# Kernel optimization log

Measured on AMD Instinct MI355X. Metric: run time of the kernel, lower is better.

Reference implementation:

```python
import jax, jax.numpy as jnp
import numpy as np


def setup_inputs() -> dict:
    key = jax.random.key(0)
    k1, k2, k3, k4 = jax.random.split(key, 4)
    B, W, S, C, h, w = 8, 5, 5, 640, 10, 10  # episodes, n_way, n_shot, channels, feat HxW
    Q = 75  # queries per episode
    return {
        "x_shot": jax.random.normal(k1, (B, W, S, C, h, w), dtype=jnp.float32),
        "x_query": jax.random.normal(k2, (B, Q, C, h, w), dtype=jnp.float32),
        "r_cos": jax.random.normal(k3, (1,), dtype=jnp.float32),
        "r_dn4": jax.random.normal(k4, (1,), dtype=jnp.float32),
        "neighbor_k": 5,
    }


def reference(x_shot, x_query, r_cos, r_dn4, neighbor_k):
    B, W, S, C, h, w = x_shot.shape
    Q = x_query.shape[1]
    hw = h * w

    base = x_shot.reshape(B, W, S, C, hw)            # [B,W,S,C,hw]
    query = x_query.reshape(B, Q, C, hw)             # [B,Q,C,hw]

    # --- cosine prototype branch ---
    base_mean = base.mean(axis=4)                    # [B,W,S,C] GAP
    proto = base_mean.mean(axis=2)                   # [B,W,C]
    q_mean = query.mean(axis=3)                      # [B,Q,C]
    qn = q_mean / jnp.linalg.norm(q_mean, axis=-1, keepdims=True)
    pn = proto / jnp.linalg.norm(proto, axis=-1, keepdims=True)
    logits_cos = jnp.einsum('bqc,bwc->bqw', qn, pn)  # [B,Q,W]

    # --- DN4 local-descriptor branch ---
    # support descriptors: [B,W,S*hw,C]
    base_mix = jnp.transpose(base, (0, 1, 2, 4, 3)).reshape(B, W, S * hw, C)
    # NOTE: original code normalizes support along the DESCRIPTOR axis (dim 0 of [S*hw,C]),
    # i.e. per-channel across descriptors. Reproduce that faithfully.
    sup = base_mix / jnp.linalg.norm(base_mix, axis=2, keepdims=True)
    # query descriptors: [B,Q,hw,C], L2-normalized per descriptor (over C)
    qd = jnp.transpose(query, (0, 1, 3, 2))
    qd = qd / jnp.linalg.norm(qd, axis=-1, keepdims=True)

    # patch-wise similarity: [B,Q,W,hw,S*hw]
    sim = jnp.einsum('bqpc,bwdc->bqwpd', qd, sup)
    topv, _ = jax.lax.top_k(sim, neighbor_k)         # [B,Q,W,hw,k]
    # original: sum over ALL (hw rows x k) top values, divided by neighbor_k
    logits_dn4 = topv.sum(axis=(-1, -2)) / neighbor_k  # [B,Q,W]

    return r_cos * logits_cos + r_dn4 * logits_dn4
```

## Files before the change

kernel.cpp:

```cpp
#include <hip/hip_runtime.h>
#include <cstddef>

typedef unsigned short u16;
typedef _Float16 f16x8 __attribute__((ext_vector_type(8)));
typedef float f32x4 __attribute__((ext_vector_type(4)));

#define NB  8
#define NW  5
#define NS  5
#define NC  640
#define NHW 100
#define NQ  75
#define ND  500
#define NDP 512
#define NR  7500
#define NRP 7552
#define NRT 59

#define OFF_SUP   ((size_t)0)
#define OFF_ABF   ((size_t)26214400)
#define OFF_QRN   ((size_t)103546880)
#define OFF_PROTO ((size_t)103788544)

__device__ __forceinline__ u16 f2h_bits(float x) {
  _Float16 h = (_Float16)x;
  return __builtin_bit_cast(u16, h);
}
__device__ __forceinline__ float h2f_bits(u16 u) {
  return (float)__builtin_bit_cast(_Float16, u);
}

__device__ __forceinline__ float block_sum(float v, float* sc, int t) {
  v += __shfl_xor(v, 32, 64);
  v += __shfl_xor(v, 16, 64);
  v += __shfl_xor(v, 8, 64);
  v += __shfl_xor(v, 4, 64);
  v += __shfl_xor(v, 2, 64);
  v += __shfl_xor(v, 1, 64);
  __syncthreads();
  if ((t & 63) == 0) sc[t >> 6] = v;
  __syncthreads();
  return sc[0] + sc[1] + sc[2] + sc[3];
}

__device__ __forceinline__ void t5_insert(float (&t5)[5], float v) {
  if (v > t5[0]) {
    t5[0] = v; float tmp;
    if (t5[0] > t5[1]) { tmp = t5[0]; t5[0] = t5[1]; t5[1] = tmp; }
    if (t5[1] > t5[2]) { tmp = t5[1]; t5[1] = t5[2]; t5[2] = tmp; }
    if (t5[2] > t5[3]) { tmp = t5[2]; t5[2] = t5[3]; t5[3] = tmp; }
    if (t5[3] > t5[4]) { tmp = t5[3]; t5[3] = t5[4]; t5[4] = tmp; }
  }
}

__global__ __launch_bounds__(256) void k1_sup(const float* __restrict__ xs,
                                              u16* __restrict__ sup2,
                                              float* __restrict__ proto_g) {
  const int cc = blockIdx.x, w = blockIdx.y, b = blockIdx.z;
  const int t = threadIdx.x;
  __shared__ u16 tile[512 * 34];
  __shared__ float rn[32];
  const size_t bw = (size_t)b * NW + w;
  const float* xbase = xs + bw * NS * NC * NHW;
  const int cb = cc * 32;

  for (int s = 0; s < NS; s++) {
    const float4* rb = (const float4*)(xbase + ((size_t)s * NC + cb) * NHW);
    for (int i4 = t; i4 < 800; i4 += 256) {
      const float4 v = rb[i4];
      const int c = i4 / 25, p4 = i4 % 25;
      const int d = s * NHW + p4 * 4;
      tile[(d    ) * 34 + c] = f2h_bits(v.x);
      tile[(d + 1) * 34 + c] = f2h_bits(v.y);
      tile[(d + 2) * 34 + c] = f2h_bits(v.z);
      tile[(d + 3) * 34 + c] = f2h_bits(v.w);
    }
  }
  if (t < 384) tile[(500 + (t >> 5)) * 34 + (t & 31)] = 0;
  __syncthreads();
  {
    const int c = t >> 3, part = t & 7;
    float ss = 0.f, sm = 0.f;
    for (int d = part; d < ND; d += 8) {
      const float x = h2f_bits(tile[d * 34 + c]);
      ss += x * x; sm += x;
    }
    ss += __shfl_xor(ss, 1, 64); ss += __shfl_xor(ss, 2, 64); ss += __shfl_xor(ss, 4, 64);
    sm += __shfl_xor(sm, 1, 64); sm += __shfl_xor(sm, 2, 64); sm += __shfl_xor(sm, 4, 64);
    if (part == 0) {
      rn[c] = 1.0f / sqrtf(ss);
      proto_g[bw * NC + cb + c] = sm;
    }
  }
  __syncthreads();
  u16* obase = sup2 + bw * NDP * NC + cb;
  for (int idx = t; idx < 512 * 32; idx += 256) {
    const int cl = idx & 31, d = idx >> 5;
    obase[(size_t)d * NC + cl] = f2h_bits(h2f_bits(tile[d * 34 + cl]) * rn[cl]);
  }
}

__global__ __launch_bounds__(256) void k2_query(const float* __restrict__ xq,
                                                const float* __restrict__ proto_g,
                                                const float* __restrict__ rcosp,
                                                u16* __restrict__ Abf,
                                                float* __restrict__ qrn,
                                                float* __restrict__ out) {
  const int q = blockIdx.x, b = blockIdx.y;
  const int t = threadIdx.x;
  __shared__ u16 tile[128 * 106];
  __shared__ float qm[NC];
  __shared__ float qs[NHW];
  __shared__ float sc[4];
  const float* xbase = xq + ((size_t)b * NQ + q) * NC * NHW;
  u16* abase = Abf + ((size_t)b * NRP + (size_t)q * NHW) * NC;

  if (t < NHW) qs[t] = 0.f;
  __syncthreads();

  for (int cc = 0; cc < 5; cc++) {
    const float4* rb = (const float4*)(xbase + (size_t)cc * 128 * NHW);
    for (int i4 = t; i4 < 3200; i4 += 256) {
      const float4 xv = rb[i4];
      const int e = i4 * 4;
      const int p = e % NHW, cl = e / NHW;
      const unsigned lo = (unsigned)f2h_bits(xv.x) | ((unsigned)f2h_bits(xv.y) << 16);
      const unsigned hi = (unsigned)f2h_bits(xv.z) | ((unsigned)f2h_bits(xv.w) << 16);
      unsigned* tw = (unsigned*)&tile[cl * 106 + p];
      tw[0] = lo; tw[1] = hi;
    }
    __syncthreads();
    if (t < 128) {
      float s = 0.f;
      const unsigned* row = (const unsigned*)&tile[t * 106];
      for (int j = 0; j < 50; j++) {
        const unsigned u = row[j];
        s += h2f_bits((u16)(u & 0xffffu)) + h2f_bits((u16)(u >> 16));
      }
      qm[cc * 128 + t] = s;
    } else if (t < 228) {
      const int p = t - 128;
      float s = 0.f;
      for (int c = 0; c < 128; c++) {
        const float x = h2f_bits(tile[c * 106 + p]);
        s += x * x;
      }
      qs[p] += s;
    }
    {
      const int c0 = t & 63, pr = t >> 6;
      for (int p = pr; p < NHW; p += 4) {
        abase[(size_t)p * NC + cc * 128 + c0]      = tile[c0 * 106 + p];
        abase[(size_t)p * NC + cc * 128 + c0 + 64] = tile[(c0 + 64) * 106 + p];
      }
    }
    __syncthreads();
  }
  if (t < NHW) qrn[(size_t)b * NRP + q * NHW + t] = 1.0f / sqrtf(qs[t]);

  float part = 0.f;
  for (int c = t; c < NC; c += 256) part += qm[c] * qm[c];
  const float qq = block_sum(part, sc, t);
  const float rcos = rcosp[0];
  for (int w = 0; w < NW; w++) {
    const float* pr_ = proto_g + ((size_t)b * NW + w) * NC;
    float dp = 0.f, pp = 0.f;
    for (int c = t; c < NC; c += 256) { const float pv = pr_[c]; dp += qm[c] * pv; pp += pv * pv; }
    dp = block_sum(dp, sc, t);
    pp = block_sum(pp, sc, t);
    if (t == 0) out[((size_t)b * NQ + q) * NW + w] = rcos * dp / sqrtf(qq * pp);
  }
  if (q == 0) {
    u16* pz = Abf + ((size_t)b * NRP + NR) * NC;
    for (int i = t; i < (NRP - NR) * NC; i += 256) pz[i] = 0;
  }
}

__global__ __launch_bounds__(256, 3) void k4_dn4(const u16* __restrict__ Abf,
                                                 const u16* __restrict__ sup2,
                                                 const float* __restrict__ qrn,
                                                 const float* __restrict__ rdn4p,
                                                 const int* __restrict__ nkp,
                                                 float* __restrict__ out) {
  const int rt = blockIdx.x, w = blockIdx.y, b = blockIdx.z;
  const int t = threadIdx.x;
  const int lane = t & 63, wid = t >> 6;
  const int m = lane & 15, quad = lane >> 4;
  const int wx = wid & 1, wy = wid >> 1;

  __shared__ __align__(16) u16 stg[2][2][128 * 40];

  const u16* Ab = Abf + ((size_t)b * NRP + (size_t)rt * 128) * NC;
  const u16* Bb = sup2 + ((size_t)b * NW + w) * NDP * NC;

  const int rr = t >> 2;
  const int c8 = (t & 3) * 8;

  uint4 ra0, ra1, rb0, rb1;

#define G_LOAD2(CT_, K0_) do {                                            \
    const u16* ap_ = Ab + (size_t)rr * NC + (K0_) + c8;                   \
    ra0 = *(const uint4*)ap_;                                             \
    ra1 = *(const uint4*)(ap_ + (size_t)64 * NC);                         \
    const u16* bp_ = Bb + (size_t)((CT_) * 128 + rr) * NC + (K0_) + c8;   \
    rb0 = *(const uint4*)bp_;                                             \
    rb1 = *(const uint4*)(bp_ + (size_t)64 * NC);                         \
  } while (0)

#define LDS_STORE(BUF_) do {                                              \
    *(uint4*)&stg[BUF_][0][rr * 40 + c8]        = ra0;                    \
    *(uint4*)&stg[BUF_][0][(rr + 64) * 40 + c8] = ra1;                    \
    *(uint4*)&stg[BUF_][1][rr * 40 + c8]        = rb0;                    \
    *(uint4*)&stg[BUF_][1][(rr + 64) * 40 + c8] = rb1;                    \
  } while (0)

  float t5[4][5];
#pragma unroll
  for (int qt = 0; qt < 4; qt++)
#pragma unroll
    for (int i = 0; i < 5; i++) t5[qt][i] = -3e38f;

  G_LOAD2(0, 0);
  LDS_STORE(0);
  G_LOAD2(0, 32);
  __syncthreads();

  for (int ct = 0; ct < 4; ct++) {
    f32x4 acc[4][4];
#pragma unroll
    for (int dt = 0; dt < 4; dt++)
#pragma unroll
      for (int qt = 0; qt < 4; qt++)
        acc[dt][qt] = (f32x4){0.f, 0.f, 0.f, 0.f};

    for (int s = 0; s < 20; s++) {
      if (!(ct == 3 && s == 19)) LDS_STORE((s + 1) & 1);
      if (!(ct == 3 && s >= 18)) {
        const int ctn = (s < 18) ? ct : ct + 1;
        const int k0n = ((s < 18) ? (s + 2) : (s - 18)) * 32;
        G_LOAD2(ctn, k0n);
      }
      {
        const u16* la = &stg[s & 1][0][0];
        const u16* lb = &stg[s & 1][1][0];
        f16x8 af0, af1, af2, af3, bf0, bf1, bf2, bf3;
        af0 = *(const f16x8*)&la[(wy * 64 +  0 + m) * 40 + quad * 8];
        af1 = *(const f16x8*)&la[(wy * 64 + 16 + m) * 40 + quad * 8];
        af2 = *(const f16x8*)&la[(wy * 64 + 32 + m) * 40 + quad * 8];
        af3 = *(const f16x8*)&la[(wy * 64 + 48 + m) * 40 + quad * 8];
        bf0 = *(const f16x8*)&lb[(wx * 64 +  0 + m) * 40 + quad * 8];
        bf1 = *(const f16x8*)&lb[(wx * 64 + 16 + m) * 40 + quad * 8];
        bf2 = *(const f16x8*)&lb[(wx * 64 + 32 + m) * 40 + quad * 8];
        bf3 = *(const f16x8*)&lb[(wx * 64 + 48 + m) * 40 + quad * 8];
        acc[0][0] = __builtin_amdgcn_mfma_f32_16x16x32_f16(bf0, af0, acc[0][0], 0, 0, 0);
        acc[0][1] = __builtin_amdgcn_mfma_f32_16x16x32_f16(bf0, af1, acc[0][1], 0, 0, 0);
        acc[0][2] = __builtin_amdgcn_mfma_f32_16x16x32_f16(bf0, af2, acc[0][2], 0, 0, 0);
        acc[0][3] = __builtin_amdgcn_mfma_f32_16x16x32_f16(bf0, af3, acc[0][3], 0, 0, 0);
        acc[1][0] = __builtin_amdgcn_mfma_f32_16x16x32_f16(bf1, af0, acc[1][0], 0, 0, 0);
        acc[1][1] = __builtin_amdgcn_mfma_f32_16x16x32_f16(bf1, af1, acc[1][1], 0, 0, 0);
        acc[1][2] = __builtin_amdgcn_mfma_f32_16x16x32_f16(bf1, af2, acc[1][2], 0, 0, 0);
        acc[1][3] = __builtin_amdgcn_mfma_f32_16x16x32_f16(bf1, af3, acc[1][3], 0, 0, 0);
        acc[2][0] = __builtin_amdgcn_mfma_f32_16x16x32_f16(bf2, af0, acc[2][0], 0, 0, 0);
        acc[2][1] = __builtin_amdgcn_mfma_f32_16x16x32_f16(bf2, af1, acc[2][1], 0, 0, 0);
        acc[2][2] = __builtin_amdgcn_mfma_f32_16x16x32_f16(bf2, af2, acc[2][2], 0, 0, 0);
        acc[2][3] = __builtin_amdgcn_mfma_f32_16x16x32_f16(bf2, af3, acc[2][3], 0, 0, 0);
        acc[3][0] = __builtin_amdgcn_mfma_f32_16x16x32_f16(bf3, af0, acc[3][0], 0, 0, 0);
        acc[3][1] = __builtin_amdgcn_mfma_f32_16x16x32_f16(bf3, af1, acc[3][1], 0, 0, 0);
        acc[3][2] = __builtin_amdgcn_mfma_f32_16x16x32_f16(bf3, af2, acc[3][2], 0, 0, 0);
        acc[3][3] = __builtin_amdgcn_mfma_f32_16x16x32_f16(bf3, af3, acc[3][3], 0, 0, 0);
      }
      __syncthreads();
    }

    const int dlim = ND - ct * 128 - wx * 64;
    if (dlim >= 64) {
#pragma unroll
      for (int dt = 0; dt < 4; dt++)
#pragma unroll
        for (int qt = 0; qt < 4; qt++)
#pragma unroll
          for (int r = 0; r < 4; r++)
            t5_insert(t5[qt], acc[dt][qt][r]);
    } else {
#pragma unroll
      for (int dt = 0; dt < 4; dt++)
#pragma unroll
        for (int qt = 0; qt < 4; qt++)
#pragma unroll
          for (int r = 0; r < 4; r++)
            if (dt * 16 + quad * 4 + r < dlim) t5_insert(t5[qt], acc[dt][qt][r]);
    }
  }

#pragma unroll
  for (int qt = 0; qt < 4; qt++) {
    float rec[5];
#pragma unroll
    for (int i = 0; i < 5; i++) rec[i] = __shfl_xor(t5[qt][i], 16, 64);
#pragma unroll
    for (int i = 0; i < 5; i++) t5_insert(t5[qt], rec[i]);
#pragma unroll
    for (int i = 0; i < 5; i++) rec[i] = __shfl_xor(t5[qt][i], 32, 64);
#pragma unroll
    for (int i = 0; i < 5; i++) t5_insert(t5[qt], rec[i]);
  }

  float* scratch = (float*)&stg[0][0][0];
  if (wx == 1 && quad == 0) {
#pragma unroll
    for (int qt = 0; qt < 4; qt++) {
      const int row = wy * 64 + qt * 16 + m;
#pragma unroll
      for (int i = 0; i < 5; i++) scratch[row * 5 + i] = t5[qt][i];
    }
  }
  __syncthreads();
  if (wx == 0 && quad == 0) {
    const float scale = rdn4p[0] / (float)nkp[0];
#pragma unroll
    for (int qt = 0; qt < 4; qt++) {
      const int row = wy * 64 + qt * 16 + m;
#pragma unroll
      for (int i = 0; i < 5; i++) t5_insert(t5[qt], scratch[row * 5 + i]);
      const int r = rt * 128 + row;
      if (r < NR) {
        const float s = t5[qt][0] + t5[qt][1] + t5[qt][2] + t5[qt][3] + t5[qt][4];
        const float contrib = s * qrn[(size_t)b * NRP + r] * scale;
        const int qi = r / NHW;
        atomicAdd(&out[((size_t)b * NQ + qi) * NW + w], contrib);
      }
    }
  }
#undef G_LOAD2
#undef LDS_STORE
}

extern "C" void kernel_launch(void* const* d_in, const int* in_sizes, int n_in,
                              void* d_out, int out_size, void* d_ws, size_t ws_size,
                              hipStream_t stream) {
  (void)in_sizes; (void)n_in; (void)out_size; (void)ws_size;
  const float* xs   = (const float*)d_in[0];
  const float* xq   = (const float*)d_in[1];
  const float* rcos = (const float*)d_in[2];
  const float* rdn4 = (const float*)d_in[3];
  const int*   nk   = (const int*)d_in[4];
  float* out = (float*)d_out;
  char* ws = (char*)d_ws;
  u16*   sup2  = (u16*)(ws + OFF_SUP);
  u16*   Abf   = (u16*)(ws + OFF_ABF);
  float* qrn   = (float*)(ws + OFF_QRN);
  float* proto = (float*)(ws + OFF_PROTO);

  k1_sup <<<dim3(20, NW, NB),  dim3(256), 0, stream>>>(xs, sup2, proto);
  k2_query<<<dim3(NQ, NB),     dim3(256), 0, stream>>>(xq, proto, rcos, Abf, qrn, out);
  k4_dn4 <<<dim3(NRT, NW, NB), dim3(256), 0, stream>>>(Abf, sup2, qrn, rdn4, nk, out);
}
```

Baseline: 508.7 us.

## Deepen global prefetch to two slabs and use fragment-ordered LDS layout

The DN4 GEMM kernel now keeps two register sets of prefetched global data, so loads run two k-slabs ahead instead of one, hiding more memory latency behind the MFMAs. The LDS staging layout also changes from a padded row-major tile (stride 40) to a linear, fragment-ordered layout. Each thread stores and reads contiguous 16-byte chunks, which removes the address arithmetic and is meant to avoid bank conflicts. The cost is extra VGPRs for the second prefetch set, which could hurt occupancy under launch_bounds(256,3).

After: 595.8 us. 1.17x slower.

```diff
diff --git a/kernel.cpp b/kernel.cpp
--- a/kernel.cpp
+++ b/kernel.cpp
@@ -188,42 +188,102 @@
   const int m = lane & 15, quad = lane >> 4;
   const int wx = wid & 1, wy = wid >> 1;
 
-  __shared__ __align__(16) u16 stg[2][2][128 * 40];
+  __shared__ __align__(16) u16 stg[2][2][4096];
 
   const u16* Ab = Abf + ((size_t)b * NRP + (size_t)rt * 128) * NC;
   const u16* Bb = sup2 + ((size_t)b * NW + w) * NDP * NC;
 
-  const int rr = t >> 2;
-  const int c8 = (t & 3) * 8;
-
-  uint4 ra0, ra1, rb0, rb1;
-
-#define G_LOAD2(CT_, K0_) do {                                            \
-    const u16* ap_ = Ab + (size_t)rr * NC + (K0_) + c8;                   \
-    ra0 = *(const uint4*)ap_;                                             \
-    ra1 = *(const uint4*)(ap_ + (size_t)64 * NC);                         \
-    const u16* bp_ = Bb + (size_t)((CT_) * 128 + rr) * NC + (K0_) + c8;   \
-    rb0 = *(const uint4*)bp_;                                             \
-    rb1 = *(const uint4*)(bp_ + (size_t)64 * NC);                         \
+  const int row0 = ((t >> 6) << 4) | (t & 15);
+  const int qc = (t >> 4) & 3;
+  const size_t aoff = (size_t)row0 * NC + qc * 8;
+  const size_t a64 = (size_t)64 * NC;
+  const int tt8 = t * 8;
+  const int lane8 = lane * 8;
+  const int wyo = wy * 2048, wxo = wx * 2048;
+
+  uint4 pA0, pA1, pB0, pB1;
+  uint4 qA0, qA1, qB0, qB1;
+
+  float t5[4][5];
+#pragma unroll
+  for (int qt = 0; qt < 4; qt++)
+#pragma unroll
+    for (int i = 0; i < 5; i++) t5[qt][i] = -3e38f;
+
+  {
+    const u16* ap = Ab + aoff;
+    pA0 = *(const uint4*)ap;
+    pA1 = *(const uint4*)(ap + a64);
+    const u16* bp = Bb + aoff;
+    pB0 = *(const uint4*)bp;
+    pB1 = *(const uint4*)(bp + a64);
+    *(uint4*)&stg[0][0][tt8]        = pA0;
+    *(uint4*)&stg[0][0][tt8 + 2048] = pA1;
+    *(uint4*)&stg[0][1][tt8]        = pB0;
+    *(uint4*)&stg[0][1][tt8 + 2048] = pB1;
+    pA0 = *(const uint4*)(ap + 32);
+    pA1 = *(const uint4*)(ap + a64 + 32);
+    pB0 = *(const uint4*)(bp + 32);
+    pB1 = *(const uint4*)(bp + a64 + 32);
+    qA0 = *(const uint4*)(ap + 64);
+    qA1 = *(const uint4*)(ap + a64 + 64);
+    qB0 = *(const uint4*)(bp + 64);
+    qB1 = *(const uint4*)(bp + a64 + 64);
+  }
+  __syncthreads();
+
+  const float* qrb = qrn + (size_t)b * NRP;
+
+#define SLAB_ITER(S_, RA0_, RA1_, RB0_, RB1_) do {                          \
+    if (!(ct == 3 && (S_) == 19)) {                                         \
+      u16* sa_ = &stg[((S_) + 1) & 1][0][0];                                \
+      *(uint4*)&sa_[tt8]        = RA0_;                                     \
+      *(uint4*)&sa_[tt8 + 2048] = RA1_;                                     \
+      u16* sb_ = &stg[((S_) + 1) & 1][1][0];                                \
+      *(uint4*)&sb_[tt8]        = RB0_;                                     \
+      *(uint4*)&sb_[tt8 + 2048] = RB1_;                                     \
+    }                                                                       \
+    if (!(ct == 3 && (S_) >= 17)) {                                         \
+      const int ct3_ = ((S_) < 17) ? ct : ct + 1;                           \
+      const int k0_  = (((S_) < 17) ? ((S_) + 3) : ((S_) - 17)) * 32;       \
+      const u16* ap_ = Ab + aoff + k0_;                                     \
+      RA0_ = *(const uint4*)ap_;                                            \
+      RA1_ = *(const uint4*)(ap_ + a64);                                    \
+      const u16* bp_ = Bb + (size_t)ct3_ * (128 * NC) + aoff + k0_;         \
+      RB0_ = *(const uint4*)bp_;                                            \
+      RB1_ = *(const uint4*)(bp_ + a64);                                    \
+    }                                                                       \
+    {                                                                       \
+      const u16* la_ = &stg[(S_) & 1][0][wyo];                              \
+      const u16* lb_ = &stg[(S_) & 1][1][wxo];                              \
+      f16x8 af0, af1, af2, af3, bf0, bf1, bf2, bf3;                         \
+      af0 = *(const f16x8*)&la_[lane8];                                     \
+      af1 = *(const f16x8*)&la_[lane8 + 512];                               \
+      af2 = *(const f16x8*)&la_[lane8 + 1024];                              \
+      af3 = *(const f16x8*)&la_[lane8 + 1536];                              \
+      bf0 = *(const f16x8*)&lb_[lane8];                                     \
+      bf1 = *(const f16x8*)&lb_[lane8 + 512];                               \
+      bf2 = *(const f16x8*)&lb_[lane8 + 1024];                              \
+      bf3 = *(const f16x8*)&lb_[lane8 + 1536];                              \
+      acc[0][0] = __builtin_amdgcn_mfma_f32_16x16x32_f16(bf0, af0, acc[0][0], 0, 0, 0); \
+      acc[0][1] = __builtin_amdgcn_mfma_f32_16x16x32_f16(bf0, af1, acc[0][1], 0, 0, 0); \
+      acc[0][2] = __builtin_amdgcn_mfma_f32_16x16x32_f16(bf0, af2, acc[0][2], 0, 0, 0); \
+      acc[0][3] = __builtin_amdgcn_mfma_f32_16x16x32_f16(bf0, af3, acc[0][3], 0, 0, 0); \
+      acc[1][0] = __builtin_amdgcn_mfma_f32_16x16x32_f16(bf1, af0, acc[1][0], 0, 0, 0); \
+      acc[1][1] = __builtin_amdgcn_mfma_f32_16x16x32_f16(bf1, af1, acc[1][1], 0, 0, 0); \
+      acc[1][2] = __builtin_amdgcn_mfma_f32_16x16x32_f16(bf1, af2, acc[1][2], 0, 0, 0); \
+      acc[1][3] = __builtin_amdgcn_mfma_f32_16x16x32_f16(bf1, af3, acc[1][3], 0, 0, 0); \
+      acc[2][0] = __builtin_amdgcn_mfma_f32_16x16x32_f16(bf2, af0, acc[2][0], 0, 0, 0); \
+      acc[2][1] = __builtin_amdgcn_mfma_f32_16x16x32_f16(bf2, af1, acc[2][1], 0, 0, 0); \
+      acc[2][2] = __builtin_amdgcn_mfma_f32_16x16x32_f16(bf2, af2, acc[2][2], 0, 0, 0); \
+      acc[2][3] = __builtin_amdgcn_mfma_f32_16x16x32_f16(bf2, af3, acc[2][3], 0, 0, 0); \
+      acc[3][0] = __builtin_amdgcn_mfma_f32_16x16x32_f16(bf3, af0, acc[3][0], 0, 0, 0); \
+      acc[3][1] = __builtin_amdgcn_mfma_f32_16x16x32_f16(bf3, af1, acc[3][1], 0, 0, 0); \
+      acc[3][2] = __builtin_amdgcn_mfma_f32_16x16x32_f16(bf3, af2, acc[3][2], 0, 0, 0); \
+      acc[3][3] = __builtin_amdgcn_mfma_f32_16x16x32_f16(bf3, af3, acc[3][3], 0, 0, 0); \
+    }                                                                       \
+    __syncthreads();                                                        \
   } while (0)
-
-#define LDS_STORE(BUF_) do {                                              \
-    *(uint4*)&stg[BUF_][0][rr * 40 + c8]        = ra0;                    \
-    *(uint4*)&stg[BUF_][0][(rr + 64) * 40 + c8] = ra1;                    \
-    *(uint4*)&stg[BUF_][1][rr * 40 + c8]        = rb0;                    \
-    *(uint4*)&stg[BUF_][1][(rr + 64) * 40 + c8] = rb1;                    \
-  } while (0)
-
-  float t5[4][5];
-#pragma unroll
-  for (int qt = 0; qt < 4; qt++)
-#pragma unroll
-    for (int i = 0; i < 5; i++) t5[qt][i] = -3e38f;
-
-  G_LOAD2(0, 0);
-  LDS_STORE(0);
-  G_LOAD2(0, 32);
-  __syncthreads();
 
   for (int ct = 0; ct < 4; ct++) {
     f32x4 acc[4][4];
@@ -233,43 +293,9 @@
       for (int qt = 0; qt < 4; qt++)
         acc[dt][qt] = (f32x4){0.f, 0.f, 0.f, 0.f};
 
-    for (int s = 0; s < 20; s++) {
-      if (!(ct == 3 && s == 19)) LDS_STORE((s + 1) & 1);
-      if (!(ct == 3 && s >= 18)) {
-        const int ctn = (s < 18) ? ct : ct + 1;
-        const int k0n = ((s < 18) ? (s + 2) : (s - 18)) * 32;
-        G_LOAD2(ctn, k0n);
-      }
-      {
-        const u16* la = &stg[s & 1][0][0];
-        const u16* lb = &stg[s & 1][1][0];
-        f16x8 af0, af1, af2, af3, bf0, bf1, bf2, bf3;
-        af0 = *(const f16x8*)&la[(wy * 64 +  0 + m) * 40 + quad * 8];
-        af1 = *(const f16x8*)&la[(wy * 64 + 16 + m) * 40 + quad * 8];
-        af2 = *(const f16x8*)&la[(wy * 64 + 32 + m) * 40 + quad * 8];
-        af3 = *(const f16x8*)&la[(wy * 64 + 48 + m) * 40 + quad * 8];
-        bf0 = *(const f16x8*)&lb[(wx * 64 +  0 + m) * 40 + quad * 8];
-        bf1 = *(const f16x8*)&lb[(wx * 64 + 16 + m) * 40 + quad * 8];
-        bf2 = *(const f16x8*)&lb[(wx * 64 + 32 + m) * 40 + quad * 8];
-        bf3 = *(const f16x8*)&lb[(wx * 64 + 48 + m) * 40 + quad * 8];
-        acc[0][0] = __builtin_amdgcn_mfma_f32_16x16x32_f16(bf0, af0, acc[0][0], 0, 0, 0);
-        acc[0][1] = __builtin_amdgcn_mfma_f32_16x16x32_f16(bf0, af1, acc[0][1], 0, 0, 0);
-        acc[0][2] = __builtin_amdgcn_mfma_f32_16x16x32_f16(bf0, af2, acc[0][2], 0, 0, 0);
-        acc[0][3] = __builtin_amdgcn_mfma_f32_16x16x32_f16(bf0, af3, acc[0][3], 0, 0, 0);
-        acc[1][0] = __builtin_amdgcn_mfma_f32_16x16x32_f16(bf1, af0, acc[1][0], 0, 0, 0);
-        acc[1][1] = __builtin_amdgcn_mfma_f32_16x16x32_f16(bf1, af1, acc[1][1], 0, 0, 0);
-        acc[1][2] = __builtin_amdgcn_mfma_f32_16x16x32_f16(bf1, af2, acc[1][2], 0, 0, 0);
-        acc[1][3] = __builtin_amdgcn_mfma_f32_16x16x32_f16(bf1, af3, acc[1][3], 0, 0, 0);
-        acc[2][0] = __builtin_amdgcn_mfma_f32_16x16x32_f16(bf2, af0, acc[2][0], 0, 0, 0);
-        acc[2][1] = __builtin_amdgcn_mfma_f32_16x16x32_f16(bf2, af1, acc[2][1], 0, 0, 0);
-        acc[2][2] = __builtin_amdgcn_mfma_f32_16x16x32_f16(bf2, af2, acc[2][2], 0, 0, 0);
-        acc[2][3] = __builtin_amdgcn_mfma_f32_16x16x32_f16(bf2, af3, acc[2][3], 0, 0, 0);
-        acc[3][0] = __builtin_amdgcn_mfma_f32_16x16x32_f16(bf3, af0, acc[3][0], 0, 0, 0);
-        acc[3][1] = __builtin_amdgcn_mfma_f32_16x16x32_f16(bf3, af1, acc[3][1], 0, 0, 0);
-        acc[3][2] = __builtin_amdgcn_mfma_f32_16x16x32_f16(bf3, af2, acc[3][2], 0, 0, 0);
-        acc[3][3] = __builtin_amdgcn_mfma_f32_16x16x32_f16(bf3, af3, acc[3][3], 0, 0, 0);
-      }
-      __syncthreads();
+    for (int s = 0; s < 20; s += 2) {
+      SLAB_ITER(s,     pA0, pA1, pB0, pB1);
+      SLAB_ITER(s + 1, qA0, qA1, qB0, qB1);
     }
 
     const int dlim = ND - ct * 128 - wx * 64;
@@ -291,6 +317,7 @@
             if (dt * 16 + quad * 4 + r < dlim) t5_insert(t5[qt], acc[dt][qt][r]);
     }
   }
+#undef SLAB_ITER
 
 #pragma unroll
   for (int qt = 0; qt < 4; qt++) {
@@ -325,14 +352,12 @@
       const int r = rt * 128 + row;
       if (r < NR) {
         const float s = t5[qt][0] + t5[qt][1] + t5[qt][2] + t5[qt][3] + t5[qt][4];
-        const float contrib = s * qrn[(size_t)b * NRP + r] * scale;
+        const float contrib = s * qrb[r] * scale;
         const int qi = r / NHW;
         atomicAdd(&out[((size_t)b * NQ + qi) * NW + w], contrib);
       }
     }
   }
-#undef G_LOAD2
-#undef LDS_STORE
 }
 
 extern "C" void kernel_launch(void* const* d_in, const int* in_sizes, int n_in,
```

## Use direct global-to-LDS loads with triple-buffered pipeline in DN4 GEMM

Applied to the files above, without the earlier changes.

Replaces the register-staged global loads and LDS stores in the DN4 similarity GEMM with global_load_lds direct-to-LDS copies. Staging becomes triple-buffered, synchronised by vmcnt waits and raw s_barrier. The LDS layout changes from padded row-major to fragment-ordered 16x32 tiles, so each lane reads its MFMA operand contiguously. This removes the VGPR staging and LDS write instructions and lets loads overlap compute more deeply, but it relies on correct vmcnt accounting. LDS use rises slightly (3x2x4096 u16 = 48 KiB).

Result: slower. 562.6 us (+10.6%).

```diff
diff --git a/kernel.cpp b/kernel.cpp
--- a/kernel.cpp
+++ b/kernel.cpp
@@ -29,6 +29,19 @@
 __device__ __forceinline__ float h2f_bits(u16 u) {
   return (float)__builtin_bit_cast(_Float16, u);
 }
+
+__device__ __forceinline__ void gload_lds16(const u16* g, u16* l) {
+  __builtin_amdgcn_global_load_lds(
+      (const __attribute__((address_space(1))) unsigned int*)g,
+      (__attribute__((address_space(3))) unsigned int*)l,
+      16, 0, 0);
+}
+
+#define S_VMCNT4() asm volatile("s_waitcnt vmcnt(4)" ::: "memory")
+#define S_VMCNT0() asm volatile("s_waitcnt vmcnt(0)" ::: "memory")
+#define S_BAR() do { __builtin_amdgcn_sched_barrier(0);          \
+                     asm volatile("s_barrier" ::: "memory");     \
+                     __builtin_amdgcn_sched_barrier(0); } while (0)
 
 __device__ __forceinline__ float block_sum(float v, float* sc, int t) {
   v += __shfl_xor(v, 32, 64);
@@ -188,43 +201,40 @@
   const int m = lane & 15, quad = lane >> 4;
   const int wx = wid & 1, wy = wid >> 1;
 
-  __shared__ __align__(16) u16 stg[2][2][128 * 40];
+  __shared__ __align__(16) u16 stg[3][2][4096];
 
   const u16* Ab = Abf + ((size_t)b * NRP + (size_t)rt * 128) * NC;
   const u16* Bb = sup2 + ((size_t)b * NW + w) * NDP * NC;
 
-  const int rr = t >> 2;
-  const int c8 = (t & 3) * 8;
-
-  uint4 ra0, ra1, rb0, rb1;
-
-#define G_LOAD2(CT_, K0_) do {                                            \
-    const u16* ap_ = Ab + (size_t)rr * NC + (K0_) + c8;                   \
-    ra0 = *(const uint4*)ap_;                                             \
-    ra1 = *(const uint4*)(ap_ + (size_t)64 * NC);                         \
-    const u16* bp_ = Bb + (size_t)((CT_) * 128 + rr) * NC + (K0_) + c8;   \
-    rb0 = *(const uint4*)bp_;                                             \
-    rb1 = *(const uint4*)(bp_ + (size_t)64 * NC);                         \
+  const size_t go0 = (size_t)(wid * 16 + m) * NC + (size_t)quad * 8;
+  const size_t go1 = (size_t)((wid + 4) * 16 + m) * NC + (size_t)quad * 8;
+  const int l0 = wid * 512 + lane * 8;
+  const int l1 = (wid + 4) * 512 + lane * 8;
+  const int lane8 = lane * 8;
+  const int wyo = wy * 2048, wxo = wx * 2048;
+
+#define ISSUE(BN_, CT_, K0_) do {                                         \
+    const size_t bO_ = (size_t)(CT_) * (128 * NC) + (K0_);                \
+    u16* s0_ = &stg[BN_][0][0];                                           \
+    u16* s1_ = &stg[BN_][1][0];                                           \
+    gload_lds16(Ab + go0 + (K0_), s0_ + l0);                              \
+    gload_lds16(Ab + go1 + (K0_), s0_ + l1);                              \
+    gload_lds16(Bb + bO_ + go0,   s1_ + l0);                              \
+    gload_lds16(Bb + bO_ + go1,   s1_ + l1);                              \
   } while (0)
 
-#define LDS_STORE(BUF_) do {                                              \
-    *(uint4*)&stg[BUF_][0][rr * 40 + c8]        = ra0;                    \
-    *(uint4*)&stg[BUF_][0][(rr + 64) * 40 + c8] = ra1;                    \
-    *(uint4*)&stg[BUF_][1][rr * 40 + c8]        = rb0;                    \
-    *(uint4*)&stg[BUF_][1][(rr + 64) * 40 + c8] = rb1;                    \
-  } while (0)
-
   float t5[4][5];
 #pragma unroll
   for (int qt = 0; qt < 4; qt++)
 #pragma unroll
     for (int i = 0; i < 5; i++) t5[qt][i] = -3e38f;
 
-  G_LOAD2(0, 0);
-  LDS_STORE(0);
-  G_LOAD2(0, 32);
-  __syncthreads();
-
+  ISSUE(0, 0, 0);
+  ISSUE(1, 0, 32);
+  S_VMCNT4();
+  S_BAR();
+
+  int bcur = 0;
   for (int ct = 0; ct < 4; ct++) {
     f32x4 acc[4][4];
 #pragma unroll
@@ -234,24 +244,24 @@
         acc[dt][qt] = (f32x4){0.f, 0.f, 0.f, 0.f};
 
     for (int s = 0; s < 20; s++) {
-      if (!(ct == 3 && s == 19)) LDS_STORE((s + 1) & 1);
+      int b2 = bcur - 1; if (b2 < 0) b2 += 3;
       if (!(ct == 3 && s >= 18)) {
         const int ctn = (s < 18) ? ct : ct + 1;
         const int k0n = ((s < 18) ? (s + 2) : (s - 18)) * 32;
-        G_LOAD2(ctn, k0n);
+        ISSUE(b2, ctn, k0n);
       }
       {
-        const u16* la = &stg[s & 1][0][0];
-        const u16* lb = &stg[s & 1][1][0];
+        const u16* la_ = &stg[bcur][0][wyo];
+        const u16* lb_ = &stg[bcur][1][wxo];
         f16x8 af0, af1, af2, af3, bf0, bf1, bf2, bf3;
-        af0 = *(const f16x8*)&la[(wy * 64 +  0 + m) * 40 + quad * 8];
-        af1 = *(const f16x8*)&la[(wy * 64 + 16 + m) * 40 + quad * 8];
-        af2 = *(const f16x8*)&la[(wy * 64 + 32 + m) * 40 + quad * 8];
-        af3 = *(const f16x8*)&la[(wy * 64 + 48 + m) * 40 + quad * 8];
-        bf0 = *(const f16x8*)&lb[(wx * 64 +  0 + m) * 40 + quad * 8];
-        bf1 = *(const f16x8*)&lb[(wx * 64 + 16 + m) * 40 + quad * 8];
-        bf2 = *(const f16x8*)&lb[(wx * 64 + 32 + m) * 40 + quad * 8];
-        bf3 = *(const f16x8*)&lb[(wx * 64 + 48 + m) * 40 + quad * 8];
+        af0 = *(const f16x8*)&la_[lane8];
+        af1 = *(const f16x8*)&la_[lane8 + 512];
+        af2 = *(const f16x8*)&la_[lane8 + 1024];
+        af3 = *(const f16x8*)&la_[lane8 + 1536];
+        bf0 = *(const f16x8*)&lb_[lane8];
+        bf1 = *(const f16x8*)&lb_[lane8 + 512];
+        bf2 = *(const f16x8*)&lb_[lane8 + 1024];
+        bf3 = *(const f16x8*)&lb_[lane8 + 1536];
         acc[0][0] = __builtin_amdgcn_mfma_f32_16x16x32_f16(bf0, af0, acc[0][0], 0, 0, 0);
         acc[0][1] = __builtin_amdgcn_mfma_f32_16x16x32_f16(bf0, af1, acc[0][1], 0, 0, 0);
         acc[0][2] = __builtin_amdgcn_mfma_f32_16x16x32_f16(bf0, af2, acc[0][2], 0, 0, 0);
@@ -269,7 +279,9 @@
         acc[3][2] = __builtin_amdgcn_mfma_f32_16x16x32_f16(bf3, af2, acc[3][2], 0, 0, 0);
         acc[3][3] = __builtin_amdgcn_mfma_f32_16x16x32_f16(bf3, af3, acc[3][3], 0, 0, 0);
       }
-      __syncthreads();
+      if (ct == 3 && s >= 18) { S_VMCNT0(); } else { S_VMCNT4(); }
+      S_BAR();
+      bcur++; if (bcur == 3) bcur = 0;
     }
 
     const int dlim = ND - ct * 128 - wx * 64;
@@ -291,6 +303,7 @@
             if (dt * 16 + quad * 4 + r < dlim) t5_insert(t5[qt], acc[dt][qt][r]);
     }
   }
+#undef ISSUE
 
 #pragma unroll
   for (int qt = 0; qt < 4; qt++) {
@@ -317,6 +330,7 @@
   __syncthreads();
   if (wx == 0 && quad == 0) {
     const float scale = rdn4p[0] / (float)nkp[0];
+    const float* qrb = qrn + (size_t)b * NRP;
 #pragma unroll
     for (int qt = 0; qt < 4; qt++) {
       const int row = wy * 64 + qt * 16 + m;
@@ -325,14 +339,12 @@
       const int r = rt * 128 + row;
       if (r < NR) {
         const float s = t5[qt][0] + t5[qt][1] + t5[qt][2] + t5[qt][3] + t5[qt][4];
-        const float contrib = s * qrn[(size_t)b * NRP + r] * scale;
+        const float contrib = s * qrb[r] * scale;
         const int qi = r / NHW;
         atomicAdd(&out[((size_t)b * NQ + qi) * NW + w], contrib);
       }
     }
   }
-#undef G_LOAD2
-#undef LDS_STORE
 }
 
 extern "C" void kernel_launch(void* const* d_in, const int* in_sizes, int n_in,
```

## Replace LDS-staged 4-wave DN4 GEMM with single-wave direct-global MFMA tiles

Applied to the files above, without the earlier changes.

The DN4 similarity kernel drops its shared-memory double-buffered 128x128 tile with four waves and __syncthreads. Each block is now one wave computing a 64-row by 128-descriptor tile, loading MFMA fragments straight from global memory. The cross-wave top-5 merge through LDS also goes away. This removes barriers and LDS traffic but gives up cross-wave operand reuse, so every fragment comes from global or L2, and the loads are strided per lane, so coalescing suffers.

Result: slower. 894.0 us (+75.7%).

```diff
diff --git a/kernel.cpp b/kernel.cpp
--- a/kernel.cpp
+++ b/kernel.cpp
@@ -15,7 +15,7 @@
 #define NDP 512
 #define NR  7500
 #define NRP 7552
-#define NRT 59
+#define NRU 118
 
 #define OFF_SUP   ((size_t)0)
 #define OFF_ABF   ((size_t)26214400)
@@ -176,43 +176,19 @@
   }
 }
 
-__global__ __launch_bounds__(256, 3) void k4_dn4(const u16* __restrict__ Abf,
-                                                 const u16* __restrict__ sup2,
-                                                 const float* __restrict__ qrn,
-                                                 const float* __restrict__ rdn4p,
-                                                 const int* __restrict__ nkp,
-                                                 float* __restrict__ out) {
-  const int rt = blockIdx.x, w = blockIdx.y, b = blockIdx.z;
-  const int t = threadIdx.x;
-  const int lane = t & 63, wid = t >> 6;
+__global__ __launch_bounds__(64, 2) void k4_dn4(const u16* __restrict__ Abf,
+                                                const u16* __restrict__ sup2,
+                                                const float* __restrict__ qrn,
+                                                const float* __restrict__ rdn4p,
+                                                const int* __restrict__ nkp,
+                                                float* __restrict__ out) {
+  const int ru = blockIdx.x, w = blockIdx.y, b = blockIdx.z;
+  const int lane = threadIdx.x & 63;
   const int m = lane & 15, quad = lane >> 4;
-  const int wx = wid & 1, wy = wid >> 1;
-
-  __shared__ __align__(16) u16 stg[2][2][128 * 40];
-
-  const u16* Ab = Abf + ((size_t)b * NRP + (size_t)rt * 128) * NC;
-  const u16* Bb = sup2 + ((size_t)b * NW + w) * NDP * NC;
-
-  const int rr = t >> 2;
-  const int c8 = (t & 3) * 8;
-
-  uint4 ra0, ra1, rb0, rb1;
-
-#define G_LOAD2(CT_, K0_) do {                                            \
-    const u16* ap_ = Ab + (size_t)rr * NC + (K0_) + c8;                   \
-    ra0 = *(const uint4*)ap_;                                             \
-    ra1 = *(const uint4*)(ap_ + (size_t)64 * NC);                         \
-    const u16* bp_ = Bb + (size_t)((CT_) * 128 + rr) * NC + (K0_) + c8;   \
-    rb0 = *(const uint4*)bp_;                                             \
-    rb1 = *(const uint4*)(bp_ + (size_t)64 * NC);                         \
-  } while (0)
-
-#define LDS_STORE(BUF_) do {                                              \
-    *(uint4*)&stg[BUF_][0][rr * 40 + c8]        = ra0;                    \
-    *(uint4*)&stg[BUF_][0][(rr + 64) * 40 + c8] = ra1;                    \
-    *(uint4*)&stg[BUF_][1][rr * 40 + c8]        = rb0;                    \
-    *(uint4*)&stg[BUF_][1][(rr + 64) * 40 + c8] = rb1;                    \
-  } while (0)
+  const int r0 = ru * 64;
+
+  const u16* Aw = Abf + ((size_t)b * NRP + r0 + m) * NC + quad * 8;
+  const u16* Bw = sup2 + (((size_t)b * NW + w) * NDP + m) * NC + quad * 8;
 
   float t5[4][5];
 #pragma unroll
@@ -220,75 +196,39 @@
 #pragma unroll
     for (int i = 0; i < 5; i++) t5[qt][i] = -3e38f;
 
-  G_LOAD2(0, 0);
-  LDS_STORE(0);
-  G_LOAD2(0, 32);
-  __syncthreads();
-
-  for (int ct = 0; ct < 4; ct++) {
-    f32x4 acc[4][4];
-#pragma unroll
-    for (int dt = 0; dt < 4; dt++)
+  for (int dc = 0; dc < 4; dc++) {
+    const u16* Bc = Bw + (size_t)dc * 128 * NC;
+    f32x4 acc[8][4];
+#pragma unroll
+    for (int dt = 0; dt < 8; dt++)
 #pragma unroll
       for (int qt = 0; qt < 4; qt++)
         acc[dt][qt] = (f32x4){0.f, 0.f, 0.f, 0.f};
 
-    for (int s = 0; s < 20; s++) {
-      if (!(ct == 3 && s == 19)) LDS_STORE((s + 1) & 1);
-      if (!(ct == 3 && s >= 18)) {
-        const int ctn = (s < 18) ? ct : ct + 1;
-        const int k0n = ((s < 18) ? (s + 2) : (s - 18)) * 32;
-        G_LOAD2(ctn, k0n);
-      }
-      {
-        const u16* la = &stg[s & 1][0][0];
-        const u16* lb = &stg[s & 1][1][0];
-        f16x8 af0, af1, af2, af3, bf0, bf1, bf2, bf3;
-        af0 = *(const f16x8*)&la[(wy * 64 +  0 + m) * 40 + quad * 8];
-        af1 = *(const f16x8*)&la[(wy * 64 + 16 + m) * 40 + quad * 8];
-        af2 = *(const f16x8*)&la[(wy * 64 + 32 + m) * 40 + quad * 8];
-        af3 = *(const f16x8*)&la[(wy * 64 + 48 + m) * 40 + quad * 8];
-        bf0 = *(const f16x8*)&lb[(wx * 64 +  0 + m) * 40 + quad * 8];
-        bf1 = *(const f16x8*)&lb[(wx * 64 + 16 + m) * 40 + quad * 8];
-        bf2 = *(const f16x8*)&lb[(wx * 64 + 32 + m) * 40 + quad * 8];
-        bf3 = *(const f16x8*)&lb[(wx * 64 + 48 + m) * 40 + quad * 8];
-        acc[0][0] = __builtin_amdgcn_mfma_f32_16x16x32_f16(bf0, af0, acc[0][0], 0, 0, 0);
-        acc[0][1] = __builtin_amdgcn_mfma_f32_16x16x32_f16(bf0, af1, acc[0][1], 0, 0, 0);
-        acc[0][2] = __builtin_amdgcn_mfma_f32_16x16x32_f16(bf0, af2, acc[0][2], 0, 0, 0);
-        acc[0][3] = __builtin_amdgcn_mfma_f32_16x16x32_f16(bf0, af3, acc[0][3], 0, 0, 0);
-        acc[1][0] = __builtin_amdgcn_mfma_f32_16x16x32_f16(bf1, af0, acc[1][0], 0, 0, 0);
-        acc[1][1] = __builtin_amdgcn_mfma_f32_16x16x32_f16(bf1, af1, acc[1][1], 0, 0, 0);
-        acc[1][2] = __builtin_amdgcn_mfma_f32_16x16x32_f16(bf1, af2, acc[1][2], 0, 0, 0);
-        acc[1][3] = __builtin_amdgcn_mfma_f32_16x16x32_f16(bf1, af3, acc[1][3], 0, 0, 0);
-        acc[2][0] = __builtin_amdgcn_mfma_f32_16x16x32_f16(bf2, af0, acc[2][0], 0, 0, 0);
-        acc[2][1] = __builtin_amdgcn_mfma_f32_16x16x32_f16(bf2, af1, acc[2][1], 0, 0, 0);
-        acc[2][2] = __builtin_amdgcn_mfma_f32_16x16x32_f16(bf2, af2, acc[2][2], 0, 0, 0);
-        acc[2][3] = __builtin_amdgcn_mfma_f32_16x16x32_f16(bf2, af3, acc[2][3], 0, 0, 0);
-        acc[3][0] = __builtin_amdgcn_mfma_f32_16x16x32_f16(bf3, af0, acc[3][0], 0, 0, 0);
-        acc[3][1] = __builtin_amdgcn_mfma_f32_16x16x32_f16(bf3, af1, acc[3][1], 0, 0, 0);
-        acc[3][2] = __builtin_amdgcn_mfma_f32_16x16x32_f16(bf3, af2, acc[3][2], 0, 0, 0);
-        acc[3][3] = __builtin_amdgcn_mfma_f32_16x16x32_f16(bf3, af3, acc[3][3], 0, 0, 0);
-      }
-      __syncthreads();
-    }
-
-    const int dlim = ND - ct * 128 - wx * 64;
-    if (dlim >= 64) {
-#pragma unroll
-      for (int dt = 0; dt < 4; dt++)
+    for (int ks = 0; ks < 20; ks++) {
+      const int k = ks * 32;
+      f16x8 af[4], bf[8];
+#pragma unroll
+      for (int qt = 0; qt < 4; qt++)
+        af[qt] = *(const f16x8*)(Aw + (size_t)qt * (16 * NC) + k);
+#pragma unroll
+      for (int dt = 0; dt < 8; dt++)
+        bf[dt] = *(const f16x8*)(Bc + (size_t)dt * (16 * NC) + k);
+#pragma unroll
+      for (int dt = 0; dt < 8; dt++)
 #pragma unroll
         for (int qt = 0; qt < 4; qt++)
-#pragma unroll
-          for (int r = 0; r < 4; r++)
-            t5_insert(t5[qt], acc[dt][qt][r]);
-    } else {
-#pragma unroll
-      for (int dt = 0; dt < 4; dt++)
-#pragma unroll
-        for (int qt = 0; qt < 4; qt++)
-#pragma unroll
-          for (int r = 0; r < 4; r++)
-            if (dt * 16 + quad * 4 + r < dlim) t5_insert(t5[qt], acc[dt][qt][r]);
+          acc[dt][qt] = __builtin_amdgcn_mfma_f32_16x16x32_f16(bf[dt], af[qt], acc[dt][qt], 0, 0, 0);
+    }
+
+#pragma unroll
+    for (int dt = 0; dt < 8; dt++) {
+      const bool tail = (dc == 3 && dt == 7);
+#pragma unroll
+      for (int qt = 0; qt < 4; qt++)
+#pragma unroll
+        for (int r = 0; r < 4; r++)
+          if (!tail || quad == 0) t5_insert(t5[qt], acc[dt][qt][r]);
     }
   }
 
@@ -305,34 +245,20 @@
     for (int i = 0; i < 5; i++) t5_insert(t5[qt], rec[i]);
   }
 
-  float* scratch = (float*)&stg[0][0][0];
-  if (wx == 1 && quad == 0) {
+  if (quad == 0) {
+    const float scale = rdn4p[0] / (float)nkp[0];
+    const float* qrb = qrn + (size_t)b * NRP;
 #pragma unroll
     for (int qt = 0; qt < 4; qt++) {
-      const int row = wy * 64 + qt * 16 + m;
-#pragma unroll
-      for (int i = 0; i < 5; i++) scratch[row * 5 + i] = t5[qt][i];
-    }
-  }
-  __syncthreads();
-  if (wx == 0 && quad == 0) {
-    const float scale = rdn4p[0] / (float)nkp[0];
-#pragma unroll
-    for (int qt = 0; qt < 4; qt++) {
-      const int row = wy * 64 + qt * 16 + m;
-#pragma unroll
-      for (int i = 0; i < 5; i++) t5_insert(t5[qt], scratch[row * 5 + i]);
-      const int r = rt * 128 + row;
+      const int r = r0 + qt * 16 + m;
       if (r < NR) {
         const float s = t5[qt][0] + t5[qt][1] + t5[qt][2] + t5[qt][3] + t5[qt][4];
-        const float contrib = s * qrn[(size_t)b * NRP + r] * scale;
+        const float contrib = s * qrb[r] * scale;
         const int qi = r / NHW;
         atomicAdd(&out[((size_t)b * NQ + qi) * NW + w], contrib);
       }
     }
   }
-#undef G_LOAD2
-#undef LDS_STORE
 }
 
 extern "C" void kernel_launch(void* const* d_in, const int* in_sizes, int n_in,
@@ -353,5 +279,5 @@
 
   k1_sup <<<dim3(20, NW, NB),  dim3(256), 0, stream>>>(xs, sup2, proto);
   k2_query<<<dim3(NQ, NB),     dim3(256), 0, stream>>>(xq, proto, rcos, Abf, qrn, out);
-  k4_dn4 <<<dim3(NRT, NW, NB), dim3(256), 0, stream>>>(Abf, sup2, qrn, rdn4, nk, out);
-}
+  k4_dn4 <<<dim3(NRU, NW, NB), dim3(64),  0, stream>>>(Abf, sup2, qrn, rdn4, nk, out);
+}
```
